# Optimization experiments

Hardware: AMD Instinct MI355X
Metric: run time of the kernel (lower is better)

Reference implementation:

```python
import jax, jax.numpy as jnp
import numpy as np

N = 100000
H = 8      # heads
C = 8      # out channels per head
NEG_SLOPE = 0.2
EPS = 1e-16


def setup_inputs() -> dict:
    key = jax.random.key(0)
    k1, k2, k3, k4, k5, k6 = jax.random.split(key, 6)
    x = jax.random.normal(k1, (N, 128), dtype=jnp.float32)
    edge_index = jax.random.randint(k2, (2, 1600000), 0, N, dtype=jnp.int64)
    W = jax.random.normal(k3, (128, H * C), dtype=jnp.float32) * (1.0 / np.sqrt(128))
    att_src = jax.random.normal(k4, (H, C), dtype=jnp.float32)
    att_dst = jax.random.normal(k5, (H, C), dtype=jnp.float32)
    bias = jax.random.normal(k6, (H * C,), dtype=jnp.float32) * 0.01
    return {"x": x, "edge_index": edge_index, "W": W,
            "att_src": att_src, "att_dst": att_dst, "bias": bias}


def _gat_forward(x, edge_index, W, att_src, att_dst, bias):
    # add self loops (PyG GATConv default add_self_loops=True)
    loop = jnp.arange(N, dtype=edge_index.dtype)
    src = jnp.concatenate([edge_index[0], loop])
    dst = jnp.concatenate([edge_index[1], loop])

    h = (x @ W).reshape(N, H, C)                       # [N,H,C]
    a_src = jnp.sum(h * att_src, axis=-1)              # [N,H]
    a_dst = jnp.sum(h * att_dst, axis=-1)              # [N,H]

    e = a_src[src] + a_dst[dst]                        # [E,H]
    e = jnp.where(e > 0, e, NEG_SLOPE * e)             # leaky_relu(0.2)

    # segment softmax over edges grouped by destination node
    m = jax.ops.segment_max(e, dst, num_segments=N)    # [N,H]
    m = jnp.where(jnp.isfinite(m), m, 0.0)
    ex = jnp.exp(e - m[dst])                           # [E,H]
    denom = jax.ops.segment_sum(ex, dst, num_segments=N)
    alpha = ex / (denom[dst] + EPS)                    # [E,H]

    msg = alpha[:, :, None] * h[src]                   # [E,H,C]
    out = jax.ops.segment_sum(msg, dst, num_segments=N)  # [N,H,C]
    out = out.reshape(N, H * C) + bias
    return jax.nn.relu(out)


def reference(x, edge_index, W, att_src, att_dst, bias):
    return _gat_forward(x, edge_index, W, att_src, att_dst, bias)
```

## Files before the change

### kernel.cpp

```cpp
#include <hip/hip_runtime.h>
#include <hip/hip_bf16.h>

#define NNODES 100000
#define NH 8
#define OUTD 64
#define FDIM 128
#define NEG_SLOPE 0.2f
#define NBUCK ((NNODES + 255) / 256)
#define MAXB 5376
#define CH 4096
#define ROWS_PB 128
#define NFB ((NNODES + ROWS_PB - 1) / ROWS_PB)
#define SHST 68

typedef __attribute__((ext_vector_type(8))) short bf16x8;
typedef __attribute__((ext_vector_type(4))) float f32x4;
typedef __attribute__((ext_vector_type(4))) unsigned int u32x4;

static __device__ __forceinline__ unsigned short f2bf(float f) {
    __hip_bfloat16 b = __float2bfloat16(f);
    return *(unsigned short*)&b;
}
static __device__ __forceinline__ float bf2f(unsigned short u) {
    __hip_bfloat16 b = *(__hip_bfloat16*)&u;
    return __bfloat162float(b);
}

__global__ void k_wprep(const float* __restrict__ W, unsigned short* __restrict__ wimg)
{
    int i = blockIdx.x * 256 + threadIdx.x;
    if (i >= FDIM * OUTD) return;
    int k = i >> 6, col = i & 63;
    int chs = (k >> 3) ^ (col & 15);
    wimg[col * FDIM + chs * 8 + (k & 7)] = f2bf(W[i]);
}

__global__ __launch_bounds__(256) void k_feat(
    const float* __restrict__ x, const unsigned short* __restrict__ wimg,
    const float* __restrict__ att_s, const float* __restrict__ att_d,
    __hip_bfloat16* __restrict__ h, float* __restrict__ asrc,
    float* __restrict__ adst)
{
    __shared__ unsigned short sx[ROWS_PB * FDIM];
    __shared__ unsigned short swt[OUTD * FDIM];
    __shared__ float shf[4 * 16 * SHST];
    __shared__ float sAs[OUTD], sAd[OUTD];

    int tid = threadIdx.x;
    if (tid < OUTD) { sAs[tid] = att_s[tid]; sAd[tid] = att_d[tid]; }

    {
        const u32x4* src = (const u32x4*)wimg;
        u32x4* dst = (u32x4*)swt;
        for (int i = tid; i < (OUTD * FDIM) / 8; i += 256) dst[i] = src[i];
    }
    int row0 = blockIdx.x * ROWS_PB;
    for (int c = tid; c < ROWS_PB * 16; c += 256) {
        int row = c >> 4, chunk = c & 15;
        int grow = row0 + row;
        unsigned short tmp[8];
        if (grow < NNODES) {
            const float* p = x + (size_t)grow * FDIM + chunk * 8;
            f32x4 f0 = *(const f32x4*)p;
            f32x4 f1 = *(const f32x4*)(p + 4);
#pragma unroll
            for (int j = 0; j < 4; ++j) tmp[j] = f2bf(f0[j]);
#pragma unroll
            for (int j = 0; j < 4; ++j) tmp[4 + j] = f2bf(f1[j]);
        } else {
#pragma unroll
            for (int j = 0; j < 8; ++j) tmp[j] = 0;
        }
        int chs = chunk ^ (row & 15);
        *(bf16x8*)&sx[row * FDIM + chs * 8] = *(bf16x8*)tmp;
    }
    __syncthreads();

    int w = tid >> 6, l = tid & 63;
    int l4 = l & 15, g = l >> 4;

    bf16x8 bfrag[16];
#pragma unroll
    for (int n = 0; n < 4; ++n)
#pragma unroll
        for (int kk = 0; kk < 4; ++kk) {
            int col = n * 16 + l4;
            int chs = (kk * 4 + g) ^ l4;
            bfrag[n * 4 + kk] = *(const bf16x8*)&swt[col * FDIM + chs * 8];
        }

    float* mysh = &shf[w * 16 * SHST];

#pragma unroll
    for (int rt = 0; rt < 2; ++rt) {
        int lbase = w * 32 + rt * 16;
        f32x4 acc[4];
#pragma unroll
        for (int n = 0; n < 4; ++n) acc[n] = (f32x4){0.f, 0.f, 0.f, 0.f};

#pragma unroll
        for (int kk = 0; kk < 4; ++kk) {
            int row = lbase + l4;
            int chs = (kk * 4 + g) ^ l4;
            bf16x8 a = *(const bf16x8*)&sx[row * FDIM + chs * 8];
#pragma unroll
            for (int n = 0; n < 4; ++n)
                acc[n] = __builtin_amdgcn_mfma_f32_16x16x32_bf16(
                    a, bfrag[n * 4 + kk], acc[n], 0, 0, 0);
        }

#pragma unroll
        for (int n = 0; n < 4; ++n)
#pragma unroll
            for (int r = 0; r < 4; ++r)
                mysh[(g * 4 + r) * SHST + n * 16 + l4] = acc[n][r];

#pragma unroll
        for (int i = 0; i < 2; ++i) {
            int c = i * 64 + l;
            int row = c >> 3, ch = c & 7;
            int grow = row0 + lbase + row;
            if (grow < NNODES) {
                const float* rp = &mysh[row * SHST + ch * 8];
                unsigned short tmp[8];
#pragma unroll
                for (int j = 0; j < 8; ++j) tmp[j] = f2bf(rp[j]);
                *(bf16x8*)&h[(size_t)grow * OUTD + ch * 8] = *(bf16x8*)tmp;
            }
        }
#pragma unroll
        for (int i = 0; i < 2; ++i) {
            int t = i * 64 + l;
            int row = t >> 3, hd = t & 7;
            int grow = row0 + lbase + row;
            if (grow < NNODES) {
                const float* rp = &mysh[row * SHST + hd * 8];
                float s1 = 0.f, s2 = 0.f;
#pragma unroll
                for (int j = 0; j < 8; ++j) {
                    s1 = fmaf(rp[j], sAs[hd * 8 + j], s1);
                    s2 = fmaf(rp[j], sAd[hd * 8 + j], s2);
                }
                asrc[grow * NH + hd] = s1;
                adst[grow * NH + hd] = s2;
            }
        }
    }
}

__global__ __launch_bounds__(256) void k_bin(
    const int* __restrict__ ei, int E, int* __restrict__ gCur,
    unsigned int* __restrict__ gSorted)
{
    __shared__ int cnt[NBUCK];
    __shared__ int base[NBUCK];
    int tot = E + NNODES;
    int e0 = blockIdx.x * CH;
    int e1 = e0 + CH; if (e1 > tot) e1 = tot;

    for (int i = threadIdx.x; i < NBUCK; i += 256) cnt[i] = 0;
    __syncthreads();

    for (int i = e0 + threadIdx.x; i < e1; i += 256) {
        int d = (i < E) ? ei[E + i] : (i - E);
        atomicAdd(&cnt[d >> 8], 1);
    }
    __syncthreads();

    for (int i = threadIdx.x; i < NBUCK; i += 256) {
        int c = cnt[i];
        base[i] = (c > 0) ? atomicAdd(&gCur[i], c) : 0;
        cnt[i] = 0;
    }
    __syncthreads();

    for (int i = e0 + threadIdx.x; i < e1; i += 256) {
        int s, d;
        if (i < E) { s = ei[i]; d = ei[E + i]; }
        else       { s = d = i - E; }
        int b = d >> 8;
        int p = base[b] + atomicAdd(&cnt[b], 1);
        if (p < MAXB)
            gSorted[(size_t)b * MAXB + p] =
                ((unsigned int)(d & 255) << 17) | (unsigned int)s;
    }
}

__global__ __launch_bounds__(256) void k_csr(
    const int* __restrict__ gCur, unsigned int* __restrict__ gSorted,
    int2* __restrict__ rows)
{
    __shared__ unsigned int ent[MAXB];
    __shared__ int cnt[256], scn[256], cur[256];
    int b = blockIdx.x;
    int n = gCur[b]; if (n > MAXB) n = MAXB;
    size_t gbase = (size_t)b * MAXB;

    for (int i = threadIdx.x; i < n; i += 256) ent[i] = gSorted[gbase + i];
    cnt[threadIdx.x] = 0;
    __syncthreads();

    for (int i = threadIdx.x; i < n; i += 256)
        atomicAdd(&cnt[ent[i] >> 17], 1);
    __syncthreads();

    int v = cnt[threadIdx.x];
    int acc = v;
    scn[threadIdx.x] = v;
    __syncthreads();
    for (int off = 1; off < 256; off <<= 1) {
        int t = (threadIdx.x >= (unsigned)off) ? scn[threadIdx.x - off] : 0;
        __syncthreads();
        acc += t;
        scn[threadIdx.x] = acc;
        __syncthreads();
    }
    int ex = acc - v;

    int node = (b << 8) + threadIdx.x;
    if (node < NNODES)
        rows[node] = make_int2((int)gbase + ex, (int)gbase + ex + v);
    cur[threadIdx.x] = ex;
    __syncthreads();

    for (int i = threadIdx.x; i < n; i += 256) {
        unsigned int p = ent[i];
        int pos = atomicAdd(&cur[p >> 17], 1);
        gSorted[gbase + pos] = p & 0x1FFFFu;
    }
}

__global__ __launch_bounds__(256) void k_gather(
    const int2* __restrict__ rows, const unsigned int* __restrict__ esrc,
    const __hip_bfloat16* __restrict__ h, const float* __restrict__ asrc,
    const float* __restrict__ adst, const float* __restrict__ bias,
    float* __restrict__ out)
{
    int node = (blockIdx.x * 256 + threadIdx.x) >> 6;
    if (node >= NNODES) return;
    int lane = threadIdx.x & 63;
    int hh = lane >> 3;

    float adh = adst[(unsigned)(node * NH + hh)];
    int2 se = rows[node];
    int start = se.x, end = se.y;
    const unsigned short* hu = (const unsigned short*)h;

    float num = 0.f, den = 0.f;
    for (int base = start; base < end; base += 64) {
        int cnt = end - base; if (cnt > 64) cnt = 64;
        int sj = (base + lane < end) ? (int)esrc[base + lane] : 0;

        int k = 0;
        for (; k + 8 <= cnt; k += 8) {
            int s0 = __builtin_amdgcn_readlane(sj, k + 0);
            int s1 = __builtin_amdgcn_readlane(sj, k + 1);
            int s2 = __builtin_amdgcn_readlane(sj, k + 2);
            int s3 = __builtin_amdgcn_readlane(sj, k + 3);
            int s4 = __builtin_amdgcn_readlane(sj, k + 4);
            int s5 = __builtin_amdgcn_readlane(sj, k + 5);
            int s6 = __builtin_amdgcn_readlane(sj, k + 6);
            int s7 = __builtin_amdgcn_readlane(sj, k + 7);
            float a0 = asrc[(unsigned)(s0 * NH + hh)];
            float a1 = asrc[(unsigned)(s1 * NH + hh)];
            float a2 = asrc[(unsigned)(s2 * NH + hh)];
            float a3 = asrc[(unsigned)(s3 * NH + hh)];
            float a4 = asrc[(unsigned)(s4 * NH + hh)];
            float a5 = asrc[(unsigned)(s5 * NH + hh)];
            float a6 = asrc[(unsigned)(s6 * NH + hh)];
            float a7 = asrc[(unsigned)(s7 * NH + hh)];
            float h0 = bf2f(hu[(unsigned)(s0 * OUTD + lane)]);
            float h1 = bf2f(hu[(unsigned)(s1 * OUTD + lane)]);
            float h2 = bf2f(hu[(unsigned)(s2 * OUTD + lane)]);
            float h3 = bf2f(hu[(unsigned)(s3 * OUTD + lane)]);
            float h4 = bf2f(hu[(unsigned)(s4 * OUTD + lane)]);
            float h5 = bf2f(hu[(unsigned)(s5 * OUTD + lane)]);
            float h6 = bf2f(hu[(unsigned)(s6 * OUTD + lane)]);
            float h7 = bf2f(hu[(unsigned)(s7 * OUTD + lane)]);
            float e0 = a0 + adh; e0 = fmaxf(e0, NEG_SLOPE * e0); e0 = __expf(e0);
            float e1 = a1 + adh; e1 = fmaxf(e1, NEG_SLOPE * e1); e1 = __expf(e1);
            float e2 = a2 + adh; e2 = fmaxf(e2, NEG_SLOPE * e2); e2 = __expf(e2);
            float e3 = a3 + adh; e3 = fmaxf(e3, NEG_SLOPE * e3); e3 = __expf(e3);
            float e4 = a4 + adh; e4 = fmaxf(e4, NEG_SLOPE * e4); e4 = __expf(e4);
            float e5 = a5 + adh; e5 = fmaxf(e5, NEG_SLOPE * e5); e5 = __expf(e5);
            float e6 = a6 + adh; e6 = fmaxf(e6, NEG_SLOPE * e6); e6 = __expf(e6);
            float e7 = a7 + adh; e7 = fmaxf(e7, NEG_SLOPE * e7); e7 = __expf(e7);
            num = fmaf(e0, h0, num); den += e0;
            num = fmaf(e1, h1, num); den += e1;
            num = fmaf(e2, h2, num); den += e2;
            num = fmaf(e3, h3, num); den += e3;
            num = fmaf(e4, h4, num); den += e4;
            num = fmaf(e5, h5, num); den += e5;
            num = fmaf(e6, h6, num); den += e6;
            num = fmaf(e7, h7, num); den += e7;
        }
        for (; k < cnt; ++k) {
            int s0 = __builtin_amdgcn_readlane(sj, k);
            float ev = asrc[(unsigned)(s0 * NH + hh)] + adh;
            ev = fmaxf(ev, NEG_SLOPE * ev);
            float ex = __expf(ev);
            float hv = bf2f(hu[(unsigned)(s0 * OUTD + lane)]);
            num = fmaf(ex, hv, num);
            den += ex;
        }
    }
    float vv = num / (den + 1e-16f) + bias[lane];
    out[(unsigned)(node * OUTD + lane)] = vv > 0.f ? vv : 0.f;
}

extern "C" void kernel_launch(void* const* d_in, const int* in_sizes, int n_in,
                              void* d_out, int out_size, void* d_ws, size_t ws_size,
                              hipStream_t stream)
{
    const float* x     = (const float*)d_in[0];
    const int*   ei    = (const int*)  d_in[1];
    const float* W     = (const float*)d_in[2];
    const float* att_s = (const float*)d_in[3];
    const float* att_d = (const float*)d_in[4];
    const float* bias  = (const float*)d_in[5];
    float* out = (float*)d_out;
    int E = in_sizes[1] / 2;
    int tot = E + NNODES;

    __hip_bfloat16* h = (__hip_bfloat16*)d_ws;
    float* asrc   = (float*)(h + (size_t)NNODES * OUTD);
    float* adst   = asrc + (size_t)NNODES * NH;
    int2*  rows   = (int2*)(adst + (size_t)NNODES * NH);
    int*   gCur   = (int*)(rows + NNODES);
    unsigned int* gSorted = (unsigned int*)(gCur + 512);
    unsigned short* wimg  = (unsigned short*)(gSorted + (size_t)NBUCK * MAXB);

    hipMemsetAsync(gCur, 0, 512 * sizeof(int), stream);

    k_wprep<<<(FDIM * OUTD + 255) / 256, 256, 0, stream>>>(W, wimg);
    k_feat<<<NFB, 256, 0, stream>>>(x, wimg, att_s, att_d, h, asrc, adst);
    k_bin<<<(tot + CH - 1) / CH, 256, 0, stream>>>(ei, E, gCur, gSorted);
    k_csr<<<NBUCK, 256, 0, stream>>>(gCur, gSorted, rows);
    k_gather<<<(NNODES * 64 + 255) / 256, 256, 0, stream>>>(
        rows, gSorted, h, asrc, adst, bias, out);
}
```

Baseline: 131.1 us.

## Process two edges per wavefront in gather using packed bf16x2 loads

The gather kernel now splits each 64-lane wavefront into two halves, each handling a different edge, with every lane loading a 32-bit word holding two bf16 channels. The halves' partial sums are combined with a cross-half shuffle before the final normalize, bias and ReLU. The aim is to halve the per-edge instruction count and serial iteration depth and to use wider loads. The cost is per-edge __shfl instead of scalar readlane for the source index, an extra reduction at the end, and a less unrolled inner loop with fewer loads in flight.

Result: faster. 125.4 us (-4.3%).

```diff
diff --git a/kernel.cpp b/kernel.cpp
--- a/kernel.cpp
+++ b/kernel.cpp
@@ -21,10 +21,6 @@
     __hip_bfloat16 b = __float2bfloat16(f);
     return *(unsigned short*)&b;
 }
-static __device__ __forceinline__ float bf2f(unsigned short u) {
-    __hip_bfloat16 b = *(__hip_bfloat16*)&u;
-    return __bfloat162float(b);
-}
 
 __global__ void k_wprep(const float* __restrict__ W, unsigned short* __restrict__ wimg)
 {
@@ -239,73 +235,61 @@
     int node = (blockIdx.x * 256 + threadIdx.x) >> 6;
     if (node >= NNODES) return;
     int lane = threadIdx.x & 63;
-    int hh = lane >> 3;
+    int l5 = lane >> 5;
+    int c  = lane & 31;
+    int hh = c >> 2;
 
     float adh = adst[(unsigned)(node * NH + hh)];
     int2 se = rows[node];
     int start = se.x, end = se.y;
-    const unsigned short* hu = (const unsigned short*)h;
-
-    float num = 0.f, den = 0.f;
+    const unsigned* hu = (const unsigned*)h;
+
+    float num0 = 0.f, num1 = 0.f, den = 0.f;
+
     for (int base = start; base < end; base += 64) {
         int cnt = end - base; if (cnt > 64) cnt = 64;
         int sj = (base + lane < end) ? (int)esrc[base + lane] : 0;
 
+        auto pair = [&](int k) {
+            int s2 = __shfl(sj, k + l5);
+            float a = asrc[(unsigned)(s2 * NH + hh)];
+            unsigned w = hu[(unsigned)(s2 * 32 + c)];
+            float e = a + adh;
+            e = fmaxf(e, NEG_SLOPE * e);
+            float ex = __expf(e);
+            den += ex;
+            union { unsigned u; float f; } lo, hi;
+            lo.u = w << 16; hi.u = w & 0xffff0000u;
+            num0 = fmaf(ex, lo.f, num0);
+            num1 = fmaf(ex, hi.f, num1);
+        };
+
         int k = 0;
-        for (; k + 8 <= cnt; k += 8) {
-            int s0 = __builtin_amdgcn_readlane(sj, k + 0);
-            int s1 = __builtin_amdgcn_readlane(sj, k + 1);
-            int s2 = __builtin_amdgcn_readlane(sj, k + 2);
-            int s3 = __builtin_amdgcn_readlane(sj, k + 3);
-            int s4 = __builtin_amdgcn_readlane(sj, k + 4);
-            int s5 = __builtin_amdgcn_readlane(sj, k + 5);
-            int s6 = __builtin_amdgcn_readlane(sj, k + 6);
-            int s7 = __builtin_amdgcn_readlane(sj, k + 7);
-            float a0 = asrc[(unsigned)(s0 * NH + hh)];
-            float a1 = asrc[(unsigned)(s1 * NH + hh)];
-            float a2 = asrc[(unsigned)(s2 * NH + hh)];
-            float a3 = asrc[(unsigned)(s3 * NH + hh)];
-            float a4 = asrc[(unsigned)(s4 * NH + hh)];
-            float a5 = asrc[(unsigned)(s5 * NH + hh)];
-            float a6 = asrc[(unsigned)(s6 * NH + hh)];
-            float a7 = asrc[(unsigned)(s7 * NH + hh)];
-            float h0 = bf2f(hu[(unsigned)(s0 * OUTD + lane)]);
-            float h1 = bf2f(hu[(unsigned)(s1 * OUTD + lane)]);
-            float h2 = bf2f(hu[(unsigned)(s2 * OUTD + lane)]);
-            float h3 = bf2f(hu[(unsigned)(s3 * OUTD + lane)]);
-            float h4 = bf2f(hu[(unsigned)(s4 * OUTD + lane)]);
-            float h5 = bf2f(hu[(unsigned)(s5 * OUTD + lane)]);
-            float h6 = bf2f(hu[(unsigned)(s6 * OUTD + lane)]);
-            float h7 = bf2f(hu[(unsigned)(s7 * OUTD + lane)]);
-            float e0 = a0 + adh; e0 = fmaxf(e0, NEG_SLOPE * e0); e0 = __expf(e0);
-            float e1 = a1 + adh; e1 = fmaxf(e1, NEG_SLOPE * e1); e1 = __expf(e1);
-            float e2 = a2 + adh; e2 = fmaxf(e2, NEG_SLOPE * e2); e2 = __expf(e2);
-            float e3 = a3 + adh; e3 = fmaxf(e3, NEG_SLOPE * e3); e3 = __expf(e3);
-            float e4 = a4 + adh; e4 = fmaxf(e4, NEG_SLOPE * e4); e4 = __expf(e4);
-            float e5 = a5 + adh; e5 = fmaxf(e5, NEG_SLOPE * e5); e5 = __expf(e5);
-            float e6 = a6 + adh; e6 = fmaxf(e6, NEG_SLOPE * e6); e6 = __expf(e6);
-            float e7 = a7 + adh; e7 = fmaxf(e7, NEG_SLOPE * e7); e7 = __expf(e7);
-            num = fmaf(e0, h0, num); den += e0;
-            num = fmaf(e1, h1, num); den += e1;
-            num = fmaf(e2, h2, num); den += e2;
-            num = fmaf(e3, h3, num); den += e3;
-            num = fmaf(e4, h4, num); den += e4;
-            num = fmaf(e5, h5, num); den += e5;
-            num = fmaf(e6, h6, num); den += e6;
-            num = fmaf(e7, h7, num); den += e7;
-        }
-        for (; k < cnt; ++k) {
-            int s0 = __builtin_amdgcn_readlane(sj, k);
-            float ev = asrc[(unsigned)(s0 * NH + hh)] + adh;
-            ev = fmaxf(ev, NEG_SLOPE * ev);
-            float ex = __expf(ev);
-            float hv = bf2f(hu[(unsigned)(s0 * OUTD + lane)]);
-            num = fmaf(ex, hv, num);
+        for (; k + 4 <= cnt; k += 4) { pair(k); pair(k + 2); }
+        for (; k + 2 <= cnt; k += 2) { pair(k); }
+        if (k < cnt) {
+            int s2 = __shfl(sj, k);
+            float a = asrc[(unsigned)(s2 * NH + hh)];
+            unsigned w = hu[(unsigned)(s2 * 32 + c)];
+            float e = a + adh;
+            e = fmaxf(e, NEG_SLOPE * e);
+            float ex = l5 ? 0.f : __expf(e);
             den += ex;
-        }
-    }
-    float vv = num / (den + 1e-16f) + bias[lane];
-    out[(unsigned)(node * OUTD + lane)] = vv > 0.f ? vv : 0.f;
+            union { unsigned u; float f; } lo, hi;
+            lo.u = w << 16; hi.u = w & 0xffff0000u;
+            num0 = fmaf(ex, lo.f, num0);
+            num1 = fmaf(ex, hi.f, num1);
+        }
+    }
+
+    num0 += __shfl_xor(num0, 32);
+    num1 += __shfl_xor(num1, 32);
+    den  += __shfl_xor(den, 32);
+
+    int ch = c * 2 + l5;
+    float inv = 1.f / (den + 1e-16f);
+    float vv = (l5 ? num1 : num0) * inv + bias[ch];
+    out[(unsigned)(node * OUTD + ch)] = vv > 0.f ? vv : 0.f;
 }
 
 extern "C" void kernel_launch(void* const* d_in, const int* in_sizes, int n_in,
```
